# Kernel tuning notes

Hardware: AMD Instinct MI355X
Metric: run time of the kernel (lower is better)

Reference implementation:

```python
import jax, jax.numpy as jnp
import numpy as np

B, H, W, C = 16, 256, 256, 3
HIDDEN, EMBED, K = 128, 64, 1024
DN = ('NHWC', 'HWIO', 'NHWC')


def _conv(x, w, b, stride):
    y = jax.lax.conv_general_dilated(x, w, (stride, stride), 'SAME', dimension_numbers=DN)
    return y + b


def _convt(x, w, b):
    y = jax.lax.conv_transpose(x, w, (2, 2), 'SAME', dimension_numbers=DN)
    return y + b


def _gelu(x):
    return jax.nn.gelu(x, approximate=True)


def setup_inputs() -> dict:
    key = jax.random.key(0)
    ks = jax.random.split(key, 12)
    wn = lambda k, shape: (jax.random.normal(k, shape, jnp.float32) * 0.02)
    return {
        'x': jax.random.normal(ks[0], (B, H, W, C), jnp.float32),
        # Encoder params
        'enc_w1': wn(ks[1], (4, 4, C, HIDDEN)), 'enc_b1': jnp.zeros((HIDDEN,), jnp.float32),
        'enc_w2': wn(ks[2], (4, 4, HIDDEN, HIDDEN)), 'enc_b2': jnp.zeros((HIDDEN,), jnp.float32),
        'enc_w3': wn(ks[3], (1, 1, HIDDEN, EMBED)), 'enc_b3': jnp.zeros((EMBED,), jnp.float32),
        # Codebook (flax uniform init: [0, scale))
        'codebook': jax.random.uniform(ks[4], (K, EMBED), jnp.float32, 0.0, 1.0),
        # Decoder params (ConvTranspose kernels are HWIO: (kh, kw, in, out))
        'dec_w1': wn(ks[5], (4, 4, EMBED, HIDDEN)), 'dec_b1': jnp.zeros((HIDDEN,), jnp.float32),
        'dec_w2': wn(ks[6], (4, 4, HIDDEN, HIDDEN)), 'dec_b2': jnp.zeros((HIDDEN,), jnp.float32),
        'dec_w3': wn(ks[7], (1, 1, HIDDEN, C)), 'dec_b3': jnp.zeros((C,), jnp.float32),
    }


def reference(x, enc_w1, enc_b1, enc_w2, enc_b2, enc_w3, enc_b3, codebook,
              dec_w1, dec_b1, dec_w2, dec_b2, dec_w3, dec_b3):
    # Encoder: two stride-2 4x4 convs + 1x1 projection to embed_dim
    h = _gelu(_conv(x, enc_w1, enc_b1, 2))
    h = _gelu(_conv(h, enc_w2, enc_b2, 2))
    z_e = _conv(h, enc_w3, enc_b3, 1)            # [B, H/4, W/4, D]

    # Vector quantization: full (BHW, K) squared-distance matrix, argmin, gather
    b, hh, ww, d = z_e.shape
    z_flat = z_e.reshape(-1, d)                   # [N, D]
    z2 = jnp.sum(z_flat ** 2, axis=1, keepdims=True)   # [N, 1]
    e2 = jnp.sum(codebook ** 2, axis=1)[None, :]        # [1, K]
    dist = z2 + e2 - 2.0 * (z_flat @ codebook.T)        # [N, K]
    idx = jnp.argmin(dist, axis=1)                      # [N]
    z_q = codebook[idx].reshape(b, hh, ww, d)

    z_st = z_e + jax.lax.stop_gradient(z_q - z_e)
    commit = jnp.mean((jax.lax.stop_gradient(z_q) - z_e) ** 2)
    codebook_loss = jnp.mean((z_q - jax.lax.stop_gradient(z_e)) ** 2)
    tok = idx.reshape(b, hh, ww)

    # Decoder: two stride-2 transposed convs + 1x1 to in_channels
    g = _gelu(_convt(z_st, dec_w1, dec_b1))
    g = _gelu(_convt(g, dec_w2, dec_b2))
    x_rec = _conv(g, dec_w3, dec_b3, 1)

    return (x_rec, tok, commit, codebook_loss)
```

## Files before the change

kernel.cpp:

```cpp
#include <hip/hip_runtime.h>
#include <math.h>


typedef __attribute__((ext_vector_type(8))) short short8;
typedef __attribute__((ext_vector_type(4))) float f32x4;

__device__ __forceinline__ float gelu_f(float x) {
    float x3 = x*x*x;
    return 0.5f*x*(1.0f + tanhf(0.7978845608028654f*(x + 0.044715f*x3)));
}
__device__ __forceinline__ float gelu_fast(float x) {
    float t = __expf(-1.5957691216057308f*(x + 0.044715f*x*x*x));
    return x / (1.f + t);
}

__device__ __forceinline__ unsigned short f2bf(float f) {
    unsigned int u = __float_as_uint(f);
    u = (u + 0x7FFFu + ((u >> 16) & 1u)) >> 16;
    return (unsigned short)u;
}
__device__ __forceinline__ float bf2f(unsigned short h) {
    return __uint_as_float(((unsigned int)h) << 16);
}

typedef const __attribute__((address_space(1))) unsigned int* gp_t;
typedef __attribute__((address_space(3))) unsigned int* lp_t;
__device__ __forceinline__ void async16(const void* g, void* l) {
    __builtin_amdgcn_global_load_lds((gp_t)g, (lp_t)l, 16, 0, 0);
}

__global__ __launch_bounds__(256) void k_conv1(const float* __restrict__ x,
        const float* __restrict__ w, const float* __restrict__ bias,
        unsigned short* __restrict__ outh, unsigned short* __restrict__ outl) {
    __shared__ __align__(16) float ws[48*128];
    __shared__ __align__(16) float xs[4][390];
    const int tid = threadIdx.x;
    const int blk = blockIdx.x;
    const int oxt = blk & 1;
    const int oy  = (blk >> 1) & 127;
    const int b   = blk >> 8;
    const int cg = tid & 15, pg = tid >> 4;
    const int c0a = cg*4, c0b = 64 + cg*4;
    const int p0 = pg*4;
    const int ox0 = oxt*64;

    for (int i = tid; i < 6144; i += 256) ws[i] = w[i];
    for (int r = 0; r < 4; ++r) {
        int iy = 2*oy + r - 1;
        bool yok = (unsigned)iy < 256u;
        const float* xrow = x + ((size_t)(b*256) + iy)*256*3;
        for (int i = tid; i < 390; i += 256) {
            int ixl = i/3, ci = i - ixl*3;
            int ix = 2*ox0 - 1 + ixl;
            xs[r][i] = (yok && (unsigned)ix < 256u) ? xrow[(size_t)ix*3 + ci] : 0.f;
        }
    }
    __syncthreads();

    float acc[4][8];
    #pragma unroll
    for (int j = 0; j < 4; ++j)
        #pragma unroll
        for (int i = 0; i < 8; ++i) acc[j][i] = 0.f;

    #pragma unroll 6
    for (int pos = 0; pos < 48; ++pos) {
        int r = pos/12, tc = pos - r*12;
        int t = tc/3,  ci = tc - t*3;
        float4 w0 = *(const float4*)&ws[pos*128 + c0a];
        float4 w1 = *(const float4*)&ws[pos*128 + c0b];
        #pragma unroll
        for (int j = 0; j < 4; ++j) {
            float av = xs[r][(2*(p0+j) + t)*3 + ci];
            acc[j][0] += av*w0.x; acc[j][1] += av*w0.y;
            acc[j][2] += av*w0.z; acc[j][3] += av*w0.w;
            acc[j][4] += av*w1.x; acc[j][5] += av*w1.y;
            acc[j][6] += av*w1.z; acc[j][7] += av*w1.w;
        }
    }
    float bv[8];
    #pragma unroll
    for (int i = 0; i < 4; ++i) { bv[i] = bias[c0a+i]; bv[4+i] = bias[c0b+i]; }
    #pragma unroll
    for (int j = 0; j < 4; ++j) {
        int ox = ox0 + p0 + j;
        size_t base = (((size_t)(b*128) + oy)*128 + ox)*128;
        ushort4 ha, hb, la, lb;
        float y;
        y = gelu_f(acc[j][0]+bv[0]); ha.x = f2bf(y); la.x = f2bf(y - bf2f(ha.x));
        y = gelu_f(acc[j][1]+bv[1]); ha.y = f2bf(y); la.y = f2bf(y - bf2f(ha.y));
        y = gelu_f(acc[j][2]+bv[2]); ha.z = f2bf(y); la.z = f2bf(y - bf2f(ha.z));
        y = gelu_f(acc[j][3]+bv[3]); ha.w = f2bf(y); la.w = f2bf(y - bf2f(ha.w));
        y = gelu_f(acc[j][4]+bv[4]); hb.x = f2bf(y); lb.x = f2bf(y - bf2f(hb.x));
        y = gelu_f(acc[j][5]+bv[5]); hb.y = f2bf(y); lb.y = f2bf(y - bf2f(hb.y));
        y = gelu_f(acc[j][6]+bv[6]); hb.z = f2bf(y); lb.z = f2bf(y - bf2f(hb.z));
        y = gelu_f(acc[j][7]+bv[7]); hb.w = f2bf(y); lb.w = f2bf(y - bf2f(hb.w));
        *(ushort4*)&outh[base + c0a] = ha;
        *(ushort4*)&outh[base + c0b] = hb;
        *(ushort4*)&outl[base + c0a] = la;
        *(ushort4*)&outl[base + c0b] = lb;
    }
}

__global__ __launch_bounds__(512) void k_conv2m(const unsigned short* __restrict__ h1h,
        const unsigned short* __restrict__ h1l,
        const unsigned short* __restrict__ w2h, const unsigned short* __restrict__ w2l,
        const float* __restrict__ bias, const float* __restrict__ zsc,
        float* __restrict__ out) {
    __shared__ __align__(16) unsigned short Ah[2*128*32];
    __shared__ __align__(16) unsigned short Al[2*128*32];
    __shared__ __align__(16) unsigned short Bh[2*128*32];
    __shared__ __align__(16) unsigned short Bl[2*128*32];
    const int tid = threadIdx.x;
    const int yy = blockIdx.x & 31;
    const int b  = blockIdx.x >> 5;
    const int oy0 = yy*2;
    const int lane = tid & 63, l15 = lane & 15, q = lane >> 4;
    const int wid = tid >> 6;
    const int wm = wid >> 1, wn = wid & 1;
    const int psub = lane >> 2;
    const int csub = (lane & 3) * 8;

    f32x4 acc[2][4];
    #pragma unroll
    for (int fm = 0; fm < 2; ++fm)
        #pragma unroll
        for (int fn = 0; fn < 4; ++fn) acc[fm][fn] = (f32x4){0.f,0.f,0.f,0.f};

    for (int tap = 0; tap < 16; ++tap) {
        int r = tap >> 2, t = tap & 3;
        for (int cs = 0; cs < 2; ++cs) {
            __syncthreads();
            #pragma unroll
            for (int j = 0; j < 8; ++j) {
                int id = wid*8 + j;
                int plane = id >> 4;
                int kc_ = (id >> 3) & 1, s2 = id & 7;
                int ci = cs*64 + kc_*32 + csub;
                if (plane < 2) {
                    int px = s2*16 + psub;
                    int oyv = oy0 + (px >> 6), ox = px & 63;
                    int iy = 2*oyv + r - 1, ix = 2*ox + t - 1;
                    bool ok = (unsigned)iy < 128u && (unsigned)ix < 128u;
                    const unsigned short* base = plane ? h1l : h1h;
                    const unsigned short* gp = ok
                        ? base + (((size_t)(b*128)+iy)*128+ix)*128 + ci
                        : (const unsigned short*)zsc;
                    async16(gp, (plane ? Al : Ah) + (kc_*128 + s2*16)*32);
                } else {
                    int co = s2*16 + psub;
                    const unsigned short* base = (plane == 3) ? w2l : w2h;
                    async16(base + ((size_t)tap*128 + co)*128 + ci,
                            ((plane == 3) ? Bl : Bh) + (kc_*128 + s2*16)*32);
                }
            }
            __syncthreads();
            #pragma unroll
            for (int kc = 0; kc < 2; ++kc) {
                short8 ah[2], al[2], bh[4], bl[4];
                #pragma unroll
                for (int fm = 0; fm < 2; ++fm) {
                    int row = (kc*128 + wm*32 + fm*16 + l15)*32 + q*8;
                    ah[fm] = *(const short8*)&Ah[row];
                    al[fm] = *(const short8*)&Al[row];
                }
                #pragma unroll
                for (int fn = 0; fn < 4; ++fn) {
                    int row = (kc*128 + wn*64 + fn*16 + l15)*32 + q*8;
                    bh[fn] = *(const short8*)&Bh[row];
                    bl[fn] = *(const short8*)&Bl[row];
                }
                #pragma unroll
                for (int fm = 0; fm < 2; ++fm)
                    #pragma unroll
                    for (int fn = 0; fn < 4; ++fn) {
                        acc[fm][fn] = __builtin_amdgcn_mfma_f32_16x16x32_bf16(
                            ah[fm], bh[fn], acc[fm][fn], 0, 0, 0);
                        acc[fm][fn] = __builtin_amdgcn_mfma_f32_16x16x32_bf16(
                            al[fm], bh[fn], acc[fm][fn], 0, 0, 0);
                        acc[fm][fn] = __builtin_amdgcn_mfma_f32_16x16x32_bf16(
                            ah[fm], bl[fn], acc[fm][fn], 0, 0, 0);
                    }
            }
        }
    }
    float bv[4];
    #pragma unroll
    for (int fn = 0; fn < 4; ++fn) bv[fn] = bias[wn*64 + fn*16 + l15];
    #pragma unroll
    for (int fm = 0; fm < 2; ++fm)
        #pragma unroll
        for (int rg = 0; rg < 4; ++rg) {
            int px = wm*32 + fm*16 + q*4 + rg;
            int oy = oy0 + (px >> 6), ox = px & 63;
            float* o = out + (((size_t)(b*64) + oy)*64 + ox)*128;
            #pragma unroll
            for (int fn = 0; fn < 4; ++fn)
                o[wn*64 + fn*16 + l15] = gelu_f(acc[fm][fn][rg] + bv[fn]);
        }
}

__global__ __launch_bounds__(256) void k_conv3(const float* __restrict__ in,
        const float* __restrict__ w, const float* __restrict__ bias,
        float* __restrict__ out) {
    __shared__ __align__(16) float xs[128*33];
    __shared__ __align__(16) float wb[32*64];
    const int tid = threadIdx.x;
    const size_t pix0 = (size_t)blockIdx.x * 128;
    const int cg = tid & 7, pg = tid >> 3;
    const int c0a = cg*4, c0b = 32 + cg*4;
    const int p0 = pg*4;

    float acc[4][8];
    #pragma unroll
    for (int j = 0; j < 4; ++j)
        #pragma unroll
        for (int i = 0; i < 8; ++i) acc[j][i] = 0.f;

    for (int cs = 0; cs < 4; ++cs) {
        __syncthreads();
        for (int i = tid; i < 4096; i += 256) {
            int p = i >> 5, ci = i & 31;
            xs[p*33 + ci] = in[(pix0 + p)*128 + cs*32 + ci];
        }
        for (int i = tid; i < 2048; i += 256) {
            int ci = i >> 6, c = i & 63;
            wb[i] = w[(size_t)(cs*32 + ci)*64 + c];
        }
        __syncthreads();
        #pragma unroll 8
        for (int ci = 0; ci < 32; ++ci) {
            float a_[4];
            #pragma unroll
            for (int j = 0; j < 4; ++j) a_[j] = xs[(p0+j)*33 + ci];
            float4 b0 = *(const float4*)&wb[ci*64 + c0a];
            float4 b1 = *(const float4*)&wb[ci*64 + c0b];
            #pragma unroll
            for (int j = 0; j < 4; ++j) {
                acc[j][0] += a_[j]*b0.x; acc[j][1] += a_[j]*b0.y;
                acc[j][2] += a_[j]*b0.z; acc[j][3] += a_[j]*b0.w;
                acc[j][4] += a_[j]*b1.x; acc[j][5] += a_[j]*b1.y;
                acc[j][6] += a_[j]*b1.z; acc[j][7] += a_[j]*b1.w;
            }
        }
    }
    #pragma unroll
    for (int j = 0; j < 4; ++j) {
        float* o = out + (pix0 + p0 + j)*64;
        float4 va, vb;
        va.x = acc[j][0]+bias[c0a+0]; va.y = acc[j][1]+bias[c0a+1];
        va.z = acc[j][2]+bias[c0a+2]; va.w = acc[j][3]+bias[c0a+3];
        vb.x = acc[j][4]+bias[c0b+0]; vb.y = acc[j][5]+bias[c0b+1];
        vb.z = acc[j][6]+bias[c0b+2]; vb.w = acc[j][7]+bias[c0b+3];
        *(float4*)&o[c0a] = va;
        *(float4*)&o[c0b] = vb;
    }
}

__global__ __launch_bounds__(256) void k_vq(const float* __restrict__ ze,
        const float* __restrict__ cb, unsigned short* __restrict__ zqb,
        float* __restrict__ tok, float* __restrict__ loss_acc) {
    __shared__ __align__(16) float zs[64*65];
    __shared__ __align__(16) float bt[64*132];
    __shared__ float es[128];
    __shared__ float z2s[64];
    __shared__ float rmin[64*16];
    __shared__ int   ridx[64*16];
    __shared__ int   widx[64];
    __shared__ float wsum[4];
    const int tid = threadIdx.x;
    const size_t tok0 = (size_t)blockIdx.x * 64;
    const int cg = tid & 15, pg = tid >> 4;
    const int k0a = cg*4, k0b = 64 + cg*4;
    const int t0 = pg*4;

    for (int i = tid; i < 4096; i += 256) {
        int tk = i >> 6, d = i & 63;
        zs[tk*65 + d] = ze[(tok0 + tk)*64 + d];
    }
    __syncthreads();
    if (tid < 64) {
        float s = 0.f;
        for (int d = 0; d < 64; ++d) { float v = zs[tid*65 + d]; s += v*v; }
        z2s[tid] = s;
    }

    float bmin[4] = {3.4e38f,3.4e38f,3.4e38f,3.4e38f};
    int   bidx[4] = {0,0,0,0};

    for (int ch = 0; ch < 8; ++ch) {
        __syncthreads();
        for (int i = tid; i < 8192; i += 256) {
            int k = i >> 6, d = i & 63;
            bt[d*132 + k] = cb[((size_t)(ch*128) + k)*64 + d];
        }
        __syncthreads();
        if (tid < 128) {
            float s = 0.f;
            for (int d = 0; d < 64; ++d) { float v = bt[d*132 + tid]; s += v*v; }
            es[tid] = s;
        }
        __syncthreads();
        float acc[4][8];
        #pragma unroll
        for (int j = 0; j < 4; ++j)
            #pragma unroll
            for (int i = 0; i < 8; ++i) acc[j][i] = 0.f;
        #pragma unroll 4
        for (int d = 0; d < 64; ++d) {
            float a_[4];
            #pragma unroll
            for (int j = 0; j < 4; ++j) a_[j] = zs[(t0+j)*65 + d];
            float4 b0 = *(const float4*)&bt[d*132 + k0a];
            float4 b1 = *(const float4*)&bt[d*132 + k0b];
            #pragma unroll
            for (int j = 0; j < 4; ++j) {
                acc[j][0] += a_[j]*b0.x; acc[j][1] += a_[j]*b0.y;
                acc[j][2] += a_[j]*b0.z; acc[j][3] += a_[j]*b0.w;
                acc[j][4] += a_[j]*b1.x; acc[j][5] += a_[j]*b1.y;
                acc[j][6] += a_[j]*b1.z; acc[j][7] += a_[j]*b1.w;
            }
        }
        #pragma unroll
        for (int j = 0; j < 4; ++j) {
            float z2 = z2s[t0+j];
            #pragma unroll
            for (int i = 0; i < 4; ++i) {
                float dist = (z2 + es[k0a+i]) - 2.f*acc[j][i];
                int idx = ch*128 + k0a + i;
                if (dist < bmin[j]) { bmin[j] = dist; bidx[j] = idx; }
            }
            #pragma unroll
            for (int i = 0; i < 4; ++i) {
                float dist = (z2 + es[k0b+i]) - 2.f*acc[j][4+i];
                int idx = ch*128 + k0b + i;
                if (dist < bmin[j]) { bmin[j] = dist; bidx[j] = idx; }
            }
        }
    }
    #pragma unroll
    for (int j = 0; j < 4; ++j) {
        rmin[(t0+j)*16 + cg] = bmin[j];
        ridx[(t0+j)*16 + cg] = bidx[j];
    }
    __syncthreads();
    if (tid < 64) {
        float bv = rmin[tid*16]; int bi = ridx[tid*16];
        for (int g = 1; g < 16; ++g) {
            float v = rmin[tid*16 + g]; int ii = ridx[tid*16 + g];
            if (v < bv || (v == bv && ii < bi)) { bv = v; bi = ii; }
        }
        widx[tid] = bi;
        tok[tok0 + tid] = (float)bi;
    }
    __syncthreads();
    float lsum = 0.f;
    for (int i = tid; i < 4096; i += 256) {
        int tk = i >> 6, d = i & 63;
        float v = cb[(size_t)widx[tk]*64 + d];
        zqb[(tok0 + tk)*64 + d] = f2bf(v);
        float diff = v - zs[tk*65 + d];
        lsum += diff*diff;
    }
    #pragma unroll
    for (int off = 32; off > 0; off >>= 1) lsum += __shfl_down(lsum, off, 64);
    if ((tid & 63) == 0) wsum[tid >> 6] = lsum;
    __syncthreads();
    if (tid == 0) atomicAdd(loss_acc, wsum[0]+wsum[1]+wsum[2]+wsum[3]);
}

__global__ __launch_bounds__(256) void k_wsplit2(const float* __restrict__ w,
        unsigned short* __restrict__ hi, unsigned short* __restrict__ lo) {
    int i = blockIdx.x*256 + threadIdx.x;
    int rt = i >> 14, rem = i & 16383;
    int co = rem >> 7, ci = rem & 127;
    float v = w[((size_t)rt*128 + ci)*128 + co];
    unsigned short h = f2bf(v);
    hi[i] = h;
    lo[i] = f2bf(v - bf2f(h));
}
__global__ __launch_bounds__(256) void k_wcvt2(const float* __restrict__ w,
        unsigned short* __restrict__ o) {
    int i = blockIdx.x*256 + threadIdx.x;
    int rt = i >> 14, rem = i & 16383;
    int co = rem >> 7, ci = rem & 127;
    o[i] = f2bf(w[((size_t)rt*128 + ci)*128 + co]);
}
__global__ __launch_bounds__(256) void k_wcvt1(const float* __restrict__ w,
        unsigned short* __restrict__ o) {
    int i = blockIdx.x*256 + threadIdx.x;
    int rt = i >> 13, rem = i & 8191;
    int co = rem >> 6, ci = rem & 63;
    o[i] = f2bf(w[((size_t)rt*64 + ci)*128 + co]);
}

__global__ __launch_bounds__(256) void k_convt1m(const unsigned short* __restrict__ zqb,
        const unsigned short* __restrict__ w1b, const float* __restrict__ bias,
        const float* __restrict__ zsc, unsigned short* __restrict__ out) {
    __shared__ __align__(16) unsigned short A[2*128*32];
    __shared__ __align__(16) unsigned short Bm[2*128*32];
    const int tid = threadIdx.x;
    const int par = blockIdx.x & 1;
    const int ey  = (blockIdx.x >> 1) & 1;
    const int qq  = (blockIdx.x >> 2) & 31;
    const int b   = blockIdx.x >> 7;
    const int q0  = qq*2;
    const int lane = tid & 63, l15 = lane & 15, q = lane >> 4;
    const int wid = tid >> 6, wm = wid >> 1, wn = wid & 1;
    const int psub = lane >> 2;
    const int csub = (lane & 3) * 8;

    f32x4 acc[4][4];
    #pragma unroll
    for (int fm = 0; fm < 4; ++fm)
        #pragma unroll
        for (int fn = 0; fn < 4; ++fn) acc[fm][fn] = (f32x4){0.f,0.f,0.f,0.f};

    for (int tap = 0; tap < 4; ++tap) {
        int rr = tap >> 1, tt = tap & 1;
        int rt = (ey + 2*rr)*4 + (par + 2*tt);
        __syncthreads();
        #pragma unroll
        for (int j = 0; j < 8; ++j) {
            int id = wid*8 + j;
            int kc = (id >> 3) & 1, s2 = id & 7;
            int ci = kc*32 + csub;
            if (id < 16) {
                int px = s2*16 + psub;
                int qv = q0 + (px >> 6), p = px & 63;
                int iy = qv + ey - 1 + rr, ix = p + par - 1 + tt;
                bool ok = (unsigned)iy < 64u && (unsigned)ix < 64u;
                const unsigned short* gp = ok
                    ? zqb + (((size_t)(b*64)+iy)*64+ix)*64 + ci
                    : (const unsigned short*)zsc;
                async16(gp, A + (kc*128 + s2*16)*32);
            } else {
                int co = s2*16 + psub;
                async16(w1b + ((size_t)rt*128 + co)*64 + ci,
                        Bm + (kc*128 + s2*16)*32);
            }
        }
        __syncthreads();
        #pragma unroll
        for (int kc = 0; kc < 2; ++kc) {
            short8 af[4], bf[4];
            #pragma unroll
            for (int fm = 0; fm < 4; ++fm)
                af[fm] = *(const short8*)&A[(kc*128 + wm*64 + fm*16 + l15)*32 + q*8];
            #pragma unroll
            for (int fn = 0; fn < 4; ++fn)
                bf[fn] = *(const short8*)&Bm[(kc*128 + wn*64 + fn*16 + l15)*32 + q*8];
            #pragma unroll
            for (int fm = 0; fm < 4; ++fm)
                #pragma unroll
                for (int fn = 0; fn < 4; ++fn)
                    acc[fm][fn] = __builtin_amdgcn_mfma_f32_16x16x32_bf16(
                        af[fm], bf[fn], acc[fm][fn], 0, 0, 0);
        }
    }
    float bv[4];
    #pragma unroll
    for (int fn = 0; fn < 4; ++fn) bv[fn] = bias[wn*64 + fn*16 + l15];
    #pragma unroll
    for (int fm = 0; fm < 4; ++fm)
        #pragma unroll
        for (int rg = 0; rg < 4; ++rg) {
            int px = wm*64 + fm*16 + q*4 + rg;
            int qv = q0 + (px >> 6), p = px & 63;
            int oy = 2*qv + ey, ox = par + 2*p;
            unsigned short* o = out + (((size_t)(b*128) + oy)*128 + ox)*128;
            #pragma unroll
            for (int fn = 0; fn < 4; ++fn)
                o[wn*64 + fn*16 + l15] = f2bf(gelu_fast(acc[fm][fn][rg] + bv[fn]));
        }
}

__global__ __launch_bounds__(512) void k_convt2(const unsigned short* __restrict__ g1b,
        const unsigned short* __restrict__ wtb, const float* __restrict__ b2,
        const float* __restrict__ w3, const float* __restrict__ b3,
        const float* __restrict__ zsc, float* __restrict__ xrec) {
    union SM {
        struct {
            unsigned short Araw[3*130*32];
            unsigned short B4[4*128*32];
        } s;
        float red[256*2*3];
    };
    __shared__ __align__(16) union SM sm;
    const int tid = threadIdx.x;
    const int gblk = blockIdx.x;
    const int xcd = gblk & 7;
    const int s_  = gblk >> 3;
    const int par = s_ & 1;
    const int qp  = (s_ >> 1) & 63;
    const int ey  = (s_ >> 7) & 1;
    const int b   = xcd*2 + (s_ >> 8);
    const int lane = tid & 63, l15 = lane & 15, q = lane >> 4;
    const int wid = tid >> 6;
    const int wm = wid >> 1, wn = wid & 1;
    const int rblk = wm >> 1;
    const int pxb  = (wm & 1)*64;
    const int ibase = 2*qp + ey - 1;

    f32x4 acc[4][4];
    #pragma unroll
    for (int fm = 0; fm < 4; ++fm)
        #pragma unroll
        for (int fn = 0; fn < 4; ++fn) acc[fm][fn] = (f32x4){0.f,0.f,0.f,0.f};

    if (tid < 24) {
        int rr = tid >> 3, rem = tid & 7, side = rem >> 2, qtr = rem & 3;
        int col = side ? 129 : 0;
        *(uint4*)&sm.s.Araw[(rr*130 + col)*32 + qtr*8] = make_uint4(0,0,0,0);
    }

    const unsigned short* aptr[3];
    int astep[3];
    unsigned int aldst[3];
    #pragma unroll
    for (int j = 0; j < 3; ++j) {
        int s0 = wid*192 + j*64;
        int rsel = s0 >> 9;
        int w0 = s0 & 511;
        int col = (w0 >> 2) + (lane >> 2);
        int iy = ibase + rsel;
        bool ok = (unsigned)iy < 128u;
        aptr[j] = ok
            ? g1b + (((size_t)(b*128) + iy)*128 + col)*128 + (lane & 3)*8
            : (const unsigned short*)zsc;
        astep[j] = ok ? 32 : 0;
        aldst[j] = (unsigned)(rsel*4160 + 32 + w0*8);
    }
    const unsigned short* bptr[4];
    unsigned int bldst[4];
    #pragma unroll
    for (int j = 0; j < 4; ++j) {
        int s0 = wid*256 + j*64;
        int tap = s0 >> 9;
        int w0 = s0 & 511;
        int co = (w0 >> 2) + (lane >> 2);
        int rr = tap >> 1, tt = tap & 1;
        int rt = (ey + 2*rr)*4 + (par + 2*tt);
        bptr[j] = wtb + ((size_t)rt*128 + co)*128 + (lane & 3)*8;
        bldst[j] = (unsigned)(tap*4096 + w0*8);
    }

    for (int kc = 0; kc < 4; ++kc) {
        __syncthreads();
        #pragma unroll
        for (int j = 0; j < 3; ++j) {
            async16(aptr[j], &sm.s.Araw[aldst[j]]);
            aptr[j] += astep[j];
        }
        #pragma unroll
        for (int j = 0; j < 4; ++j) {
            async16(bptr[j], &sm.s.B4[bldst[j]]);
            bptr[j] += 32;
        }
        __syncthreads();
        #pragma unroll
        for (int tap = 0; tap < 4; ++tap) {
            int rr = tap >> 1, tt = tap & 1;
            short8 af[4], bf[4];
            #pragma unroll
            for (int fm = 0; fm < 4; ++fm)
                af[fm] = *(const short8*)&sm.s.Araw[
                    ((rblk + rr)*130 + pxb + fm*16 + l15 + par + tt)*32 + q*8];
            #pragma unroll
            for (int fn = 0; fn < 4; ++fn)
                bf[fn] = *(const short8*)&sm.s.B4[
                    (tap*128 + wn*64 + fn*16 + l15)*32 + q*8];
            #pragma unroll
            for (int fm = 0; fm < 4; ++fm)
                #pragma unroll
                for (int fn = 0; fn < 4; ++fn)
                    acc[fm][fn] = __builtin_amdgcn_mfma_f32_16x16x32_bf16(
                        af[fm], bf[fn], acc[fm][fn], 0, 0, 0);
        }
    }

    float b2v[4];
    float w3v[4][3];
    #pragma unroll
    for (int fn = 0; fn < 4; ++fn) {
        int co = wn*64 + fn*16 + l15;
        b2v[fn] = b2[co];
        w3v[fn][0] = w3[co*3+0]; w3v[fn][1] = w3[co*3+1]; w3v[fn][2] = w3[co*3+2];
    }
    __syncthreads();
    #pragma unroll
    for (int fm = 0; fm < 4; ++fm) {
        #pragma unroll
        for (int rg = 0; rg < 4; ++rg) {
            float s0 = 0.f, s1 = 0.f, s2 = 0.f;
            #pragma unroll
            for (int fn = 0; fn < 4; ++fn) {
                float y = gelu_fast(acc[fm][fn][rg] + b2v[fn]);
                s0 += y*w3v[fn][0]; s1 += y*w3v[fn][1]; s2 += y*w3v[fn][2];
            }
            #pragma unroll
            for (int m = 1; m < 16; m <<= 1) {
                s0 += __shfl_xor(s0, m, 64);
                s1 += __shfl_xor(s1, m, 64);
                s2 += __shfl_xor(s2, m, 64);
            }
            if (l15 == 0) {
                int px256 = wm*64 + fm*16 + q*4 + rg;
                sm.red[(px256*2 + wn)*3 + 0] = s0;
                sm.red[(px256*2 + wn)*3 + 1] = s1;
                sm.red[(px256*2 + wn)*3 + 2] = s2;
            }
        }
    }
    __syncthreads();
    for (int o = tid; o < 768; o += 512) {
        int px256 = o/3, jj = o - px256*3;
        int rb = px256 >> 7, px = px256 & 127;
        int oy = 2*(2*qp + rb) + ey;
        float s = b3[jj] + sm.red[(px256*2 + 0)*3 + jj] + sm.red[(px256*2 + 1)*3 + jj];
        xrec[(((size_t)(b*256) + oy)*256 + (par + 2*px))*3 + jj] = s;
    }
}

__global__ void k_zero(float* lacc, float* zsc) {
    if (threadIdx.x == 0) lacc[0] = 0.f;
    if (threadIdx.x < 4) zsc[threadIdx.x] = 0.f;
}

__global__ void k_finalize(const float* __restrict__ loss_acc, float* __restrict__ o) {
    if (threadIdx.x == 0) {
        float v = loss_acc[0] * (1.0f/4194304.0f);
        o[0] = v;
        o[1] = v;
    }
}

extern "C" void kernel_launch(void* const* d_in, const int* in_sizes, int n_in,
                              void* d_out, int out_size, void* d_ws, size_t ws_size,
                              hipStream_t stream) {
    (void)in_sizes; (void)n_in; (void)out_size; (void)ws_size;
    const float* x   = (const float*)d_in[0];
    const float* ew1 = (const float*)d_in[1];
    const float* eb1 = (const float*)d_in[2];
    const float* ew2 = (const float*)d_in[3];
    const float* eb2 = (const float*)d_in[4];
    const float* ew3 = (const float*)d_in[5];
    const float* eb3 = (const float*)d_in[6];
    const float* cb  = (const float*)d_in[7];
    const float* dw1 = (const float*)d_in[8];
    const float* db1 = (const float*)d_in[9];
    const float* dw2 = (const float*)d_in[10];
    const float* db2 = (const float*)d_in[11];
    const float* dw3 = (const float*)d_in[12];
    const float* db3 = (const float*)d_in[13];

    float* ws = (float*)d_ws;
    unsigned short* h1h  = (unsigned short*)(ws);
    unsigned short* h1l  = (unsigned short*)(ws + 16777216);
    float*          h2   = ws + 33554432;
    float*          ze   = ws + 41943040;
    unsigned short* zqb  = (unsigned short*)(ws + 46137344);
    unsigned short* we2h = (unsigned short*)(ws + 48234496);
    unsigned short* we2l = (unsigned short*)(ws + 48365568);
    unsigned short* wd2b = (unsigned short*)(ws + 48496640);
    unsigned short* wd1b = (unsigned short*)(ws + 48627712);
    float*          lacc = ws + 48693248;
    float*          zsc  = ws + 48693252;
    unsigned short* g1b  = h1h;

    float* xrec = (float*)d_out;
    float* tokf = xrec + 3145728;
    float* loss = tokf + 65536;

    k_zero    <<<   1,  64, 0, stream>>>(lacc, zsc);
    k_wsplit2 <<<1024, 256, 0, stream>>>(ew2, we2h, we2l);
    k_wcvt2   <<<1024, 256, 0, stream>>>(dw2, wd2b);
    k_wcvt1   <<< 512, 256, 0, stream>>>(dw1, wd1b);
    k_conv1   <<<4096, 256, 0, stream>>>(x, ew1, eb1, h1h, h1l);
    k_conv2m  <<< 512, 512, 0, stream>>>(h1h, h1l, we2h, we2l, eb2, zsc, h2);
    k_conv3   <<< 512, 256, 0, stream>>>(h2, ew3, eb3, ze);
    k_vq      <<<1024, 256, 0, stream>>>(ze, cb, zqb, tokf, lacc);
    k_convt1m <<<4096, 256, 0, stream>>>(zqb, wd1b, db1, zsc, g1b);
    k_convt2  <<<4096, 512, 0, stream>>>(g1b, wd2b, db2, dw3, db3, zsc, xrec);
    k_finalize<<<   1,  64, 0, stream>>>(lacc, loss);
}
```

Measured before the change: 725.2 us.

## Move VQ distance search onto split-bf16 MFMA and enlarge convt1 tiles

The vector-quantization distance GEMM moves from scalar FP32 FMAs to bf16 MFMA. It uses a hi/lo split of both z_e and the codebook (three MFMAs per tile) to keep near-FP32 accuracy. Codebook norms and the split codebook are precomputed in separate small kernels, and conv3 now also emits split bf16 copies of z_e. Separately, the first transposed-conv kernel is retiled to 512 threads covering four rows per block, which reuses the weight tile across more pixels. The split-bf16 arithmetic carries some risk of argmin ties or flips compared with the FP32 reference.

```diff
diff --git a/kernel.cpp b/kernel.cpp
--- a/kernel.cpp
+++ b/kernel.cpp
@@ -202,7 +202,8 @@
 
 __global__ __launch_bounds__(256) void k_conv3(const float* __restrict__ in,
         const float* __restrict__ w, const float* __restrict__ bias,
-        float* __restrict__ out) {
+        float* __restrict__ out, unsigned short* __restrict__ outzh,
+        unsigned short* __restrict__ outzl) {
     __shared__ __align__(16) float xs[128*33];
     __shared__ __align__(16) float wb[32*64];
     const int tid = threadIdx.x;
@@ -246,120 +247,175 @@
     }
     #pragma unroll
     for (int j = 0; j < 4; ++j) {
-        float* o = out + (pix0 + p0 + j)*64;
-        float4 va, vb;
-        va.x = acc[j][0]+bias[c0a+0]; va.y = acc[j][1]+bias[c0a+1];
-        va.z = acc[j][2]+bias[c0a+2]; va.w = acc[j][3]+bias[c0a+3];
-        vb.x = acc[j][4]+bias[c0b+0]; vb.y = acc[j][5]+bias[c0b+1];
-        vb.z = acc[j][6]+bias[c0b+2]; vb.w = acc[j][7]+bias[c0b+3];
-        *(float4*)&o[c0a] = va;
-        *(float4*)&o[c0b] = vb;
-    }
-}
-
-__global__ __launch_bounds__(256) void k_vq(const float* __restrict__ ze,
-        const float* __restrict__ cb, unsigned short* __restrict__ zqb,
-        float* __restrict__ tok, float* __restrict__ loss_acc) {
-    __shared__ __align__(16) float zs[64*65];
-    __shared__ __align__(16) float bt[64*132];
-    __shared__ float es[128];
-    __shared__ float z2s[64];
-    __shared__ float rmin[64*16];
-    __shared__ int   ridx[64*16];
-    __shared__ int   widx[64];
+        size_t base = (pix0 + p0 + j)*64;
+        float v[8];
+        #pragma unroll
+        for (int i = 0; i < 4; ++i) { v[i] = acc[j][i]+bias[c0a+i]; v[4+i] = acc[j][4+i]+bias[c0b+i]; }
+        float4 va = make_float4(v[0],v[1],v[2],v[3]);
+        float4 vb = make_float4(v[4],v[5],v[6],v[7]);
+        *(float4*)&out[base + c0a] = va;
+        *(float4*)&out[base + c0b] = vb;
+        ushort4 ha, la, hb, lb;
+        ha.x = f2bf(v[0]); la.x = f2bf(v[0]-bf2f(ha.x));
+        ha.y = f2bf(v[1]); la.y = f2bf(v[1]-bf2f(ha.y));
+        ha.z = f2bf(v[2]); la.z = f2bf(v[2]-bf2f(ha.z));
+        ha.w = f2bf(v[3]); la.w = f2bf(v[3]-bf2f(ha.w));
+        hb.x = f2bf(v[4]); lb.x = f2bf(v[4]-bf2f(hb.x));
+        hb.y = f2bf(v[5]); lb.y = f2bf(v[5]-bf2f(hb.y));
+        hb.z = f2bf(v[6]); lb.z = f2bf(v[6]-bf2f(hb.z));
+        hb.w = f2bf(v[7]); lb.w = f2bf(v[7]-bf2f(hb.w));
+        *(ushort4*)&outzh[base + c0a] = ha;
+        *(ushort4*)&outzh[base + c0b] = hb;
+        *(ushort4*)&outzl[base + c0a] = la;
+        *(ushort4*)&outzl[base + c0b] = lb;
+    }
+}
+
+__global__ __launch_bounds__(256) void k_wsplitcb(const float* __restrict__ cb,
+        unsigned short* __restrict__ hi, unsigned short* __restrict__ lo) {
+    int i = blockIdx.x*256 + threadIdx.x;
+    float v = cb[i];
+    unsigned short h = f2bf(v);
+    hi[i] = h;
+    lo[i] = f2bf(v - bf2f(h));
+}
+__global__ __launch_bounds__(256) void k_e2(const float* __restrict__ cb,
+        float* __restrict__ e2g) {
+    int k = blockIdx.x*256 + threadIdx.x;
+    float s = 0.f;
+    for (int d = 0; d < 64; ++d) { float v = cb[(size_t)k*64 + d]; s += v*v; }
+    e2g[k] = s;
+}
+
+__global__ __launch_bounds__(256) void k_vqm(const unsigned short* __restrict__ zh,
+        const unsigned short* __restrict__ zl, const unsigned short* __restrict__ cbh,
+        const unsigned short* __restrict__ cbl, const float* __restrict__ e2g,
+        const float* __restrict__ ze, const float* __restrict__ cb,
+        unsigned short* __restrict__ zqb, float* __restrict__ tok,
+        float* __restrict__ loss_acc) {
+    __shared__ __align__(16) unsigned short Ah[2*128*32];
+    __shared__ __align__(16) unsigned short Al[2*128*32];
+    __shared__ __align__(16) unsigned short Bh[2*128*32];
+    __shared__ __align__(16) unsigned short Bl[2*128*32];
+    __shared__ float es[1024];
+    __shared__ float cval[128*2];
+    __shared__ int   cidx[128*2];
+    __shared__ int   widx[128];
     __shared__ float wsum[4];
     const int tid = threadIdx.x;
-    const size_t tok0 = (size_t)blockIdx.x * 64;
-    const int cg = tid & 15, pg = tid >> 4;
-    const int k0a = cg*4, k0b = 64 + cg*4;
-    const int t0 = pg*4;
-
-    for (int i = tid; i < 4096; i += 256) {
-        int tk = i >> 6, d = i & 63;
-        zs[tk*65 + d] = ze[(tok0 + tk)*64 + d];
-    }
-    __syncthreads();
-    if (tid < 64) {
-        float s = 0.f;
-        for (int d = 0; d < 64; ++d) { float v = zs[tid*65 + d]; s += v*v; }
-        z2s[tid] = s;
-    }
-
-    float bmin[4] = {3.4e38f,3.4e38f,3.4e38f,3.4e38f};
-    int   bidx[4] = {0,0,0,0};
+    const size_t tok0 = (size_t)blockIdx.x * 128;
+    const int lane = tid & 63, l15 = lane & 15, q = lane >> 4;
+    const int wid = tid >> 6, wm = wid >> 1, wn = wid & 1;
+    const int psub = lane >> 2, csub = (lane & 3)*8;
+
+    #pragma unroll
+    for (int j = 0; j < 8; ++j) {
+        int id = wid*8 + j;
+        int pl = id >> 4;
+        int kc = (id >> 3) & 1, s2 = id & 7;
+        const unsigned short* src = (pl ? zl : zh)
+            + (tok0 + s2*16 + psub)*64 + kc*32 + csub;
+        async16(src, (pl ? Al : Ah) + (kc*128 + s2*16)*32);
+    }
+    for (int i = tid; i < 1024; i += 256) es[i] = e2g[i];
+
+    float best[4][4];
+    int   bidx[4][4];
+    #pragma unroll
+    for (int fm = 0; fm < 4; ++fm)
+        #pragma unroll
+        for (int rg = 0; rg < 4; ++rg) { best[fm][rg] = 3.4e38f; bidx[fm][rg] = 0; }
 
     for (int ch = 0; ch < 8; ++ch) {
         __syncthreads();
-        for (int i = tid; i < 8192; i += 256) {
-            int k = i >> 6, d = i & 63;
-            bt[d*132 + k] = cb[((size_t)(ch*128) + k)*64 + d];
+        #pragma unroll
+        for (int j = 0; j < 8; ++j) {
+            int id = wid*8 + j;
+            int pl = id >> 4;
+            int kc = (id >> 3) & 1, s2 = id & 7;
+            const unsigned short* src = (pl ? cbl : cbh)
+                + ((size_t)(ch*128) + s2*16 + psub)*64 + kc*32 + csub;
+            async16(src, (pl ? Bl : Bh) + (kc*128 + s2*16)*32);
         }
         __syncthreads();
-        if (tid < 128) {
-            float s = 0.f;
-            for (int d = 0; d < 64; ++d) { float v = bt[d*132 + tid]; s += v*v; }
-            es[tid] = s;
-        }
-        __syncthreads();
-        float acc[4][8];
-        #pragma unroll
-        for (int j = 0; j < 4; ++j)
-            #pragma unroll
-            for (int i = 0; i < 8; ++i) acc[j][i] = 0.f;
-        #pragma unroll 4
-        for (int d = 0; d < 64; ++d) {
-            float a_[4];
-            #pragma unroll
-            for (int j = 0; j < 4; ++j) a_[j] = zs[(t0+j)*65 + d];
-            float4 b0 = *(const float4*)&bt[d*132 + k0a];
-            float4 b1 = *(const float4*)&bt[d*132 + k0b];
-            #pragma unroll
-            for (int j = 0; j < 4; ++j) {
-                acc[j][0] += a_[j]*b0.x; acc[j][1] += a_[j]*b0.y;
-                acc[j][2] += a_[j]*b0.z; acc[j][3] += a_[j]*b0.w;
-                acc[j][4] += a_[j]*b1.x; acc[j][5] += a_[j]*b1.y;
-                acc[j][6] += a_[j]*b1.z; acc[j][7] += a_[j]*b1.w;
-            }
-        }
-        #pragma unroll
-        for (int j = 0; j < 4; ++j) {
-            float z2 = z2s[t0+j];
-            #pragma unroll
-            for (int i = 0; i < 4; ++i) {
-                float dist = (z2 + es[k0a+i]) - 2.f*acc[j][i];
-                int idx = ch*128 + k0a + i;
-                if (dist < bmin[j]) { bmin[j] = dist; bidx[j] = idx; }
-            }
-            #pragma unroll
-            for (int i = 0; i < 4; ++i) {
-                float dist = (z2 + es[k0b+i]) - 2.f*acc[j][4+i];
-                int idx = ch*128 + k0b + i;
-                if (dist < bmin[j]) { bmin[j] = dist; bidx[j] = idx; }
-            }
-        }
-    }
-    #pragma unroll
-    for (int j = 0; j < 4; ++j) {
-        rmin[(t0+j)*16 + cg] = bmin[j];
-        ridx[(t0+j)*16 + cg] = bidx[j];
-    }
+        f32x4 acc[4][4];
+        #pragma unroll
+        for (int fm = 0; fm < 4; ++fm)
+            #pragma unroll
+            for (int fn = 0; fn < 4; ++fn) acc[fm][fn] = (f32x4){0.f,0.f,0.f,0.f};
+        #pragma unroll
+        for (int kc = 0; kc < 2; ++kc) {
+            short8 ah[4], al[4], bh[4], bl[4];
+            #pragma unroll
+            for (int fm = 0; fm < 4; ++fm) {
+                int row = (kc*128 + wm*64 + fm*16 + l15)*32 + q*8;
+                ah[fm] = *(const short8*)&Ah[row];
+                al[fm] = *(const short8*)&Al[row];
+            }
+            #pragma unroll
+            for (int fn = 0; fn < 4; ++fn) {
+                int row = (kc*128 + wn*64 + fn*16 + l15)*32 + q*8;
+                bh[fn] = *(const short8*)&Bh[row];
+                bl[fn] = *(const short8*)&Bl[row];
+            }
+            #pragma unroll
+            for (int fm = 0; fm < 4; ++fm)
+                #pragma unroll
+                for (int fn = 0; fn < 4; ++fn) {
+                    acc[fm][fn] = __builtin_amdgcn_mfma_f32_16x16x32_bf16(
+                        ah[fm], bh[fn], acc[fm][fn], 0, 0, 0);
+                    acc[fm][fn] = __builtin_amdgcn_mfma_f32_16x16x32_bf16(
+                        al[fm], bh[fn], acc[fm][fn], 0, 0, 0);
+                    acc[fm][fn] = __builtin_amdgcn_mfma_f32_16x16x32_bf16(
+                        ah[fm], bl[fn], acc[fm][fn], 0, 0, 0);
+                }
+        }
+        #pragma unroll
+        for (int fm = 0; fm < 4; ++fm)
+            #pragma unroll
+            for (int fn = 0; fn < 4; ++fn) {
+                int code = ch*128 + wn*64 + fn*16 + l15;
+                float e2v = es[code];
+                #pragma unroll
+                for (int rg = 0; rg < 4; ++rg) {
+                    float sc = e2v - 2.f*acc[fm][fn][rg];
+                    if (sc < best[fm][rg]) { best[fm][rg] = sc; bidx[fm][rg] = code; }
+                }
+            }
+    }
+
+    #pragma unroll
+    for (int fm = 0; fm < 4; ++fm)
+        #pragma unroll
+        for (int rg = 0; rg < 4; ++rg) {
+            float bv = best[fm][rg]; int bi = bidx[fm][rg];
+            #pragma unroll
+            for (int m = 1; m < 16; m <<= 1) {
+                float ov = __shfl_xor(bv, m, 64);
+                int   oi = __shfl_xor(bi, m, 64);
+                if (ov < bv || (ov == bv && oi < bi)) { bv = ov; bi = oi; }
+            }
+            if (l15 == 0) {
+                int t = wm*64 + fm*16 + q*4 + rg;
+                cval[t*2 + wn] = bv;
+                cidx[t*2 + wn] = bi;
+            }
+        }
     __syncthreads();
-    if (tid < 64) {
-        float bv = rmin[tid*16]; int bi = ridx[tid*16];
-        for (int g = 1; g < 16; ++g) {
-            float v = rmin[tid*16 + g]; int ii = ridx[tid*16 + g];
-            if (v < bv || (v == bv && ii < bi)) { bv = v; bi = ii; }
-        }
+    if (tid < 128) {
+        float v0 = cval[tid*2], v1 = cval[tid*2 + 1];
+        int   i0 = cidx[tid*2], i1 = cidx[tid*2 + 1];
+        int bi = (v1 < v0) ? i1 : i0;
         widx[tid] = bi;
         tok[tok0 + tid] = (float)bi;
     }
     __syncthreads();
     float lsum = 0.f;
-    for (int i = tid; i < 4096; i += 256) {
+    for (int i = tid; i < 8192; i += 256) {
         int tk = i >> 6, d = i & 63;
         float v = cb[(size_t)widx[tk]*64 + d];
         zqb[(tok0 + tk)*64 + d] = f2bf(v);
-        float diff = v - zs[tk*65 + d];
+        float diff = v - ze[(tok0 + tk)*64 + d];
         lsum += diff*diff;
     }
     #pragma unroll
@@ -394,17 +450,17 @@
     o[i] = f2bf(w[((size_t)rt*64 + ci)*128 + co]);
 }
 
-__global__ __launch_bounds__(256) void k_convt1m(const unsigned short* __restrict__ zqb,
+__global__ __launch_bounds__(512) void k_convt1m(const unsigned short* __restrict__ zqb,
         const unsigned short* __restrict__ w1b, const float* __restrict__ bias,
         const float* __restrict__ zsc, unsigned short* __restrict__ out) {
-    __shared__ __align__(16) unsigned short A[2*128*32];
+    __shared__ __align__(16) unsigned short A[2*256*32];
     __shared__ __align__(16) unsigned short Bm[2*128*32];
     const int tid = threadIdx.x;
     const int par = blockIdx.x & 1;
     const int ey  = (blockIdx.x >> 1) & 1;
-    const int qq  = (blockIdx.x >> 2) & 31;
-    const int b   = blockIdx.x >> 7;
-    const int q0  = qq*2;
+    const int qt  = (blockIdx.x >> 2) & 15;
+    const int b   = blockIdx.x >> 6;
+    const int q0  = qt*4;
     const int lane = tid & 63, l15 = lane & 15, q = lane >> 4;
     const int wid = tid >> 6, wm = wid >> 1, wn = wid & 1;
     const int psub = lane >> 2;
@@ -421,22 +477,23 @@
         int rt = (ey + 2*rr)*4 + (par + 2*tt);
         __syncthreads();
         #pragma unroll
-        for (int j = 0; j < 8; ++j) {
-            int id = wid*8 + j;
-            int kc = (id >> 3) & 1, s2 = id & 7;
-            int ci = kc*32 + csub;
-            if (id < 16) {
+        for (int j = 0; j < 6; ++j) {
+            int id = wid*6 + j;
+            if (id < 32) {
+                int kc = id >> 4, s2 = id & 15;
                 int px = s2*16 + psub;
                 int qv = q0 + (px >> 6), p = px & 63;
                 int iy = qv + ey - 1 + rr, ix = p + par - 1 + tt;
                 bool ok = (unsigned)iy < 64u && (unsigned)ix < 64u;
                 const unsigned short* gp = ok
-                    ? zqb + (((size_t)(b*64)+iy)*64+ix)*64 + ci
+                    ? zqb + (((size_t)(b*64)+iy)*64+ix)*64 + kc*32 + csub
                     : (const unsigned short*)zsc;
-                async16(gp, A + (kc*128 + s2*16)*32);
+                async16(gp, A + (kc*256 + s2*16)*32);
             } else {
+                int idb = id - 32;
+                int kc = idb >> 3, s2 = idb & 7;
                 int co = s2*16 + psub;
-                async16(w1b + ((size_t)rt*128 + co)*64 + ci,
+                async16(w1b + ((size_t)rt*128 + co)*64 + kc*32 + csub,
                         Bm + (kc*128 + s2*16)*32);
             }
         }
@@ -446,7 +503,7 @@
             short8 af[4], bf[4];
             #pragma unroll
             for (int fm = 0; fm < 4; ++fm)
-                af[fm] = *(const short8*)&A[(kc*128 + wm*64 + fm*16 + l15)*32 + q*8];
+                af[fm] = *(const short8*)&A[(kc*256 + wm*64 + fm*16 + l15)*32 + q*8];
             #pragma unroll
             for (int fn = 0; fn < 4; ++fn)
                 bf[fn] = *(const short8*)&Bm[(kc*128 + wn*64 + fn*16 + l15)*32 + q*8];
@@ -666,7 +723,12 @@
     unsigned short* wd1b = (unsigned short*)(ws + 48627712);
     float*          lacc = ws + 48693248;
     float*          zsc  = ws + 48693252;
+    unsigned short* cbh  = (unsigned short*)(ws + 48693264);
+    unsigned short* cbl  = (unsigned short*)(ws + 48726032);
+    float*          e2g  = ws + 48758800;
     unsigned short* g1b  = h1h;
+    unsigned short* zh   = (unsigned short*)(ws + 16777216);
+    unsigned short* zl   = (unsigned short*)(ws + 18874368);
 
     float* xrec = (float*)d_out;
     float* tokf = xrec + 3145728;
@@ -676,11 +738,13 @@
     k_wsplit2 <<<1024, 256, 0, stream>>>(ew2, we2h, we2l);
     k_wcvt2   <<<1024, 256, 0, stream>>>(dw2, wd2b);
     k_wcvt1   <<< 512, 256, 0, stream>>>(dw1, wd1b);
+    k_wsplitcb<<< 256, 256, 0, stream>>>(cb, cbh, cbl);
+    k_e2      <<<   4, 256, 0, stream>>>(cb, e2g);
     k_conv1   <<<4096, 256, 0, stream>>>(x, ew1, eb1, h1h, h1l);
     k_conv2m  <<< 512, 512, 0, stream>>>(h1h, h1l, we2h, we2l, eb2, zsc, h2);
-    k_conv3   <<< 512, 256, 0, stream>>>(h2, ew3, eb3, ze);
-    k_vq      <<<1024, 256, 0, stream>>>(ze, cb, zqb, tokf, lacc);
-    k_convt1m <<<4096, 256, 0, stream>>>(zqb, wd1b, db1, zsc, g1b);
+    k_conv3   <<< 512, 256, 0, stream>>>(h2, ew3, eb3, ze, zh, zl);
+    k_vqm     <<< 512, 256, 0, stream>>>(zh, zl, cbh, cbl, e2g, ze, cb, zqb, tokf, lacc);
+    k_convt1m <<<1024, 512, 0, stream>>>(zqb, wd1b, db1, zsc, g1b);
     k_convt2  <<<4096, 512, 0, stream>>>(g1b, wd2b, db2, dw3, db3, zsc, xrec);
     k_finalize<<<   1,  64, 0, stream>>>(lacc, loss);
 }
```

After: 589.1 us. 18.8% less time.
